# Optimization experiments

Hardware: AMD Instinct MI355X
Metric: run time of the kernel (lower is better)

Reference implementation:

```python
import jax, jax.numpy as jnp
import numpy as np

N_HEADS = 16
NEG = -1000000000.0  # masked_fill value from the original code


def setup_inputs() -> dict:
    key = jax.random.key(0)
    ks = jax.random.split(key, 7)
    D = 1024
    x = jax.random.normal(ks[0], (2, 2048, D), dtype=jnp.float32)
    s = 1.0 / np.sqrt(D)
    Wq = jax.random.normal(ks[1], (D, D), dtype=jnp.float32) * s
    bq = jax.random.normal(ks[2], (D,), dtype=jnp.float32) * 0.01
    Wk = jax.random.normal(ks[3], (D, D), dtype=jnp.float32) * s
    bk = jax.random.normal(ks[4], (D,), dtype=jnp.float32) * 0.01
    Wv = jax.random.normal(ks[5], (D, D), dtype=jnp.float32) * s
    bv = jax.random.normal(ks[6], (D,), dtype=jnp.float32) * 0.01
    return {"x": x, "Wq": Wq, "bq": bq, "Wk": Wk, "bk": bk, "Wv": Wv, "bv": bv}


def reference(x, Wq, bq, Wk, bk, Wv, bv):
    B, S, D = x.shape
    H = N_HEADS
    dh = D // H
    # nn.Linear: x @ W.T + b
    Q = (x @ Wq.T + bq).reshape(B, S, H, dh)
    K = (x @ Wk.T + bk).reshape(B, S, H, dh)
    V = (x @ Wv.T + bv).reshape(B, S, H, dh)
    # NOTE: original scales by sqrt(n_heads), not sqrt(d_head) -- faithful.
    scale = jnp.asarray(H, x.dtype) ** 0.5
    scores = jnp.einsum('bqhd,bkhd->bhqk', Q, K) / scale  # [B,H,S,S]
    # Original: mask = triu(ones, diag=1); scores.masked_fill(mask == 0, -1e9)
    # i.e. positions where the STRICT-UPPER mask is False (lower triangle incl.
    # diagonal) get -1e9. Faithful reproduction of that (buggy) behavior.
    triu = jnp.triu(jnp.ones((S, S), dtype=bool), k=1)  # [S,S]
    scores = jnp.where(triu[None, None, :, :], scores, jnp.asarray(NEG, x.dtype))
    probs = jax.nn.softmax(scores, axis=-1)
    # dropout is identity at inference
    out = jnp.einsum('bhqk,bkhd->bqhd', probs, V).reshape(B, S, D)
    return out
```

## Files before the change

### kernel.cpp

```cpp
#include <hip/hip_runtime.h>
#include <stdint.h>

typedef unsigned short u16;
typedef __attribute__((ext_vector_type(8))) short bf16x8;
typedef __attribute__((ext_vector_type(4))) float floatx4;

#define MFMA16(a, b, c) __builtin_amdgcn_mfma_f32_16x16x32_bf16(a, b, c, 0, 0, 0)
#define MEMFENCE asm volatile("" ::: "memory")

#if __has_builtin(__builtin_amdgcn_exp2f)
#define EXP2(x) __builtin_amdgcn_exp2f(x)
#else
#define EXP2(x) __expf(0.6931471805599453f * (x))
#endif

__device__ __forceinline__ u16 f2bf(float f) {
  unsigned u = __builtin_bit_cast(unsigned, f);
  return (u16)((u + 0x7FFFu + ((u >> 16) & 1u)) >> 16);
}
__device__ __forceinline__ u16 f2bf_hu(float f) {
  return (u16)((__builtin_bit_cast(unsigned, f) + 0x8000u) >> 16);
}
__device__ __forceinline__ float bf2f(u16 v) {
  return __builtin_bit_cast(float, (unsigned)v << 16);
}

__device__ __forceinline__ void glds16(void* lds, const void* g) {
  __builtin_amdgcn_global_load_lds((const __attribute__((address_space(1))) void*)g,
                                   (__attribute__((address_space(3))) void*)lds,
                                   16, 0, 0);
}

__global__ __launch_bounds__(256) void cvt_all(
    const float* __restrict__ x, const float* __restrict__ w0,
    const float* __restrict__ w1, const float* __restrict__ w2,
    u16* __restrict__ xb, u16* __restrict__ Wb) {
  const int bid = blockIdx.x;
  const float* src;
  u16* dst;
  int i;
  if (bid < 4096) {
    src = x; dst = xb; i = bid * 256 + threadIdx.x;
  } else {
    const int z = (bid - 4096) >> 10;
    src = (z == 0) ? w0 : (z == 1) ? w1 : w2;
    dst = Wb + (size_t)z * (1024 * 1024);
    i = ((bid - 4096) & 1023) * 256 + threadIdx.x;
  }
  float4 f = reinterpret_cast<const float4*>(src)[i];
  ushort4 o;
  o.x = f2bf(f.x); o.y = f2bf(f.y); o.z = f2bf(f.z); o.w = f2bf(f.w);
  reinterpret_cast<ushort4*>(dst)[i] = o;
}

__global__ __launch_bounds__(256, 3) void qkv_gemm(
    const u16* __restrict__ xb, const u16* __restrict__ Wb,
    const float* __restrict__ bq, const float* __restrict__ bk,
    const float* __restrict__ bv,
    u16* __restrict__ Qb, u16* __restrict__ Kb, u16* __restrict__ VTb) {
  __shared__ __attribute__((aligned(16))) u16 smem[2 * 128 * 64];
  u16* As = smem;
  u16* Bs = smem + 128 * 64;

  const int tid = threadIdx.x;
  const int w = tid >> 6, lane = tid & 63;
  const int lo = lane & 15, quad = lane >> 4;
  const int which = blockIdx.z;
  const int m0 = blockIdx.x * 128, n0 = blockIdx.y * 128;

  const u16* W = Wb + (size_t)which * (1024 * 1024);
  const int wm = (w >> 1) * 64, wn = (w & 1) * 64;

  floatx4 acc[4][4];
  for (int i = 0; i < 4; ++i)
    for (int j = 0; j < 4; ++j) acc[i][j] = (floatx4)0.f;

  const int arow = lane >> 3;
  const int aswz = ((lane & 7) ^ arow) * 8;

  for (int kt = 0; kt < 16; ++kt) {
    const int k0 = kt * 64;
    for (int j = 0; j < 4; ++j) {
      const int seg = w * 4 + j;
      glds16(As + seg * 512, xb + (size_t)(m0 + seg * 8 + arow) * 1024 + k0 + aswz);
      glds16(Bs + seg * 512, W + (size_t)(n0 + seg * 8 + arow) * 1024 + k0 + aswz);
    }
    __syncthreads();
    for (int kk = 0; kk < 2; ++kk) {
      const int swz = ((kk * 4 + quad) ^ (lo & 7)) * 8;
      bf16x8 af[4], bfr[4];
      for (int it = 0; it < 4; ++it)
        af[it] = *reinterpret_cast<const bf16x8*>(As + (wm + it * 16 + lo) * 64 + swz);
      for (int jt = 0; jt < 4; ++jt)
        bfr[jt] = *reinterpret_cast<const bf16x8*>(Bs + (wn + jt * 16 + lo) * 64 + swz);
      for (int it = 0; it < 4; ++it)
        for (int jt = 0; jt < 4; ++jt)
          acc[it][jt] = MFMA16(af[it], bfr[jt], acc[it][jt]);
    }
    __syncthreads();
  }

  const float* bias = (which == 0) ? bq : (which == 1) ? bk : bv;
  float bb[4];
  for (int jt = 0; jt < 4; ++jt) bb[jt] = bias[n0 + wn + jt * 16 + lo];
  const int b = m0 >> 11;

  if (which < 2) {
    const float scl = (which == 0) ? 0.36067376022224085f : 1.0f;
    u16* Tw = smem + w * (16 * 72);
    const int hblk = (n0 + wn) >> 6;
    u16* dst = ((which == 0) ? Qb : Kb) +
               ((size_t)(b * 16 + hblk) * 2048 + ((m0 & 2047) + wm)) * 64;
    for (int it = 0; it < 4; ++it) {
      for (int jt = 0; jt < 4; ++jt)
        for (int r = 0; r < 4; ++r) {
          const int m = quad * 4 + r, col = jt * 16 + lo;
          Tw[m * 72 + (((col >> 3) ^ (m & 7)) * 8) + (col & 7)] =
              f2bf((acc[it][jt][r] + bb[jt]) * scl);
        }
      MEMFENCE;
      for (int rd = 0; rd < 2; ++rd) {
        const int sr = rd * 8 + (lane >> 3), d8 = lane & 7;
        bf16x8 v = *reinterpret_cast<const bf16x8*>(Tw + sr * 72 + ((d8 ^ (sr & 7)) * 8));
        *reinterpret_cast<bf16x8*>(dst + (size_t)(it * 16 + sr) * 64 + d8 * 8) = v;
      }
      MEMFENCE;
    }
  } else {
    for (int pass = 0; pass < 2; ++pass) {
      if ((wm >> 6) == pass) {
        for (int it = 0; it < 4; ++it)
          for (int jt = 0; jt < 4; ++jt)
            for (int r = 0; r < 4; ++r) {
              const int n = wn + jt * 16 + lo;
              const int m = it * 16 + quad * 4 + r;
              smem[n * 72 + (((m >> 3) ^ (n & 7)) * 8) + (m & 7)] =
                  f2bf(acc[it][jt][r] + bb[jt]);
            }
      }
      __syncthreads();
      for (int rd = 0; rd < 4; ++rd) {
        const int n = (tid >> 3) + rd * 32, m8 = tid & 7;
        bf16x8 v = *reinterpret_cast<const bf16x8*>(smem + n * 72 + ((m8 ^ (n & 7)) * 8));
        const int ng = n0 + n, h = ng >> 6, d = ng & 63;
        const int s = (m0 & 2047) + pass * 64 + m8 * 8;
        *reinterpret_cast<bf16x8*>(VTb + ((size_t)(b * 16 + h) * 64 + d) * 2048 + s) = v;
      }
      __syncthreads();
    }
  }
}

__global__ __launch_bounds__(256, 4) void attn(
    const u16* __restrict__ Qb, const u16* __restrict__ Kb,
    const u16* __restrict__ VTb, float* __restrict__ out) {
  __shared__ __attribute__((aligned(16))) u16 Ks[2][64 * 64];
  __shared__ __attribute__((aligned(16))) u16 Vs[2][64 * 64];
  __shared__ __attribute__((aligned(16))) u16 Pt[4][16 * 64];

  const int L = blockIdx.x;
  const int bh = L & 31;
  const int j = L >> 5;
  const int g = j >> 3, r = j & 7;
  const int qi = (g == 0) ? r : (g == 1) ? 15 - r : (g == 2) ? 16 + r : 31 - r;
  const int kstart = qi;

  const int tid = threadIdx.x, w = tid >> 6, lane = tid & 63;
  const int lo = lane & 15, quad = lane >> 4;

  const u16* Qh = Qb + (size_t)bh * (2048 * 64);
  const u16* Kh = Kb + (size_t)bh * (2048 * 64);
  const u16* Vh = VTb + (size_t)bh * (64 * 2048);

  const int qrow = qi * 64 + w * 16 + lo;
  bf16x8 qf[2];
  qf[0] = *reinterpret_cast<const bf16x8*>(Qh + (size_t)qrow * 64 + quad * 8);
  qf[1] = *reinterpret_cast<const bf16x8*>(Qh + (size_t)qrow * 64 + 32 + quad * 8);

  float lrun = 0.f;
  floatx4 acc[4];
  for (int dt = 0; dt < 4; ++dt) acc[dt] = (floatx4)0.f;

  const int srow8 = lane >> 3, sblk = lane & 7;
  const int sswz = (sblk ^ srow8) * 8;

  for (int jj = 0; jj < 2; ++jj) {
    const int b8 = (w * 2 + jj) * 8;
    glds16(&Ks[0][b8 * 64], Kh + (size_t)(kstart * 64 + b8 + srow8) * 64 + sswz);
    glds16(&Vs[0][b8 * 64], Vh + (size_t)(b8 + srow8) * 2048 + kstart * 64 + sswz);
  }
  __syncthreads();

  for (int kt = kstart; kt < 32; ++kt) {
    const int cur = (kt - kstart) & 1, nxt = cur ^ 1;
    if (kt < 31)
      for (int jj = 0; jj < 2; ++jj) {
        const int b8 = (w * 2 + jj) * 8;
        glds16(&Ks[nxt][b8 * 64], Kh + (size_t)((kt + 1) * 64 + b8 + srow8) * 64 + sswz);
        glds16(&Vs[nxt][b8 * 64], Vh + (size_t)(b8 + srow8) * 2048 + (kt + 1) * 64 + sswz);
      }
    const u16* ksb = Ks[cur];
    const u16* vsb = Vs[cur];

    const bool maskp = (kt == kstart);

    floatx4 sc[4];
    for (int t = 0; t < 4; ++t) sc[t] = (floatx4)0.f;
    for (int kk = 0; kk < 2; ++kk) {
      const int swz = ((kk * 4 + quad) ^ (lo & 7)) * 8;
      for (int t = 0; t < 4; ++t) {
        bf16x8 ka = *reinterpret_cast<const bf16x8*>(ksb + (t * 16 + lo) * 64 + swz);
        sc[t] = MFMA16(ka, qf[kk], sc[t]);
      }
    }

    u16* ptw = &Pt[w][0];
    for (int t = 0; t < 4; ++t) {
      float p0 = EXP2(sc[t][0]), p1 = EXP2(sc[t][1]);
      float p2 = EXP2(sc[t][2]), p3 = EXP2(sc[t][3]);
      if (maskp) {
        const int key = kt * 64 + t * 16 + quad * 4;
        p0 = (key + 0 > qrow) ? p0 : 0.f;
        p1 = (key + 1 > qrow) ? p1 : 0.f;
        p2 = (key + 2 > qrow) ? p2 : 0.f;
        p3 = (key + 3 > qrow) ? p3 : 0.f;
      }
      lrun += (p0 + p1) + (p2 + p3);
      ushort4 pk;
      pk.x = f2bf_hu(p0); pk.y = f2bf_hu(p1);
      pk.z = f2bf_hu(p2); pk.w = f2bf_hu(p3);
      u16* pdst = ptw + lo * 64 +
                  (((2 * t + (quad >> 1)) ^ (lo & 7)) * 8) + (quad & 1) * 4;
      *reinterpret_cast<ushort4*>(pdst) = pk;
    }
    MEMFENCE;

    for (int kk = 0; kk < 2; ++kk) {
      const int pswz = ((kk * 4 + quad) ^ (lo & 7)) * 8;
      bf16x8 pb = *reinterpret_cast<const bf16x8*>(ptw + lo * 64 + pswz);
      for (int dt = 0; dt < 4; ++dt) {
        bf16x8 va = *reinterpret_cast<const bf16x8*>(vsb + (dt * 16 + lo) * 64 + pswz);
        acc[dt] = MFMA16(va, pb, acc[dt]);
      }
    }
    MEMFENCE;
    __syncthreads();
  }

  const int b = bh >> 4, hh = bh & 15;
  float l = lrun;
  l += __shfl_xor(l, 16);
  l += __shfl_xor(l, 32);
  if (l != 0.f) {
    const float rl = 1.f / l;
    float* op = out + ((size_t)(b * 2048 + qrow)) * 1024 + hh * 64 + quad * 4;
    for (int dt = 0; dt < 4; ++dt) {
      float4 o4;
      o4.x = acc[dt][0] * rl; o4.y = acc[dt][1] * rl;
      o4.z = acc[dt][2] * rl; o4.w = acc[dt][3] * rl;
      *reinterpret_cast<float4*>(op + dt * 16) = o4;
    }
  }
}

__global__ __launch_bounds__(256) void fix2047(const u16* __restrict__ VTb,
                                               float* __restrict__ out) {
  const int bh = blockIdx.x;
  const u16* Vh = VTb + (size_t)bh * (64 * 2048);
  const int t = threadIdx.x;
  const int d = t >> 2, j = t & 3;
  float s = 0.f;
  const u16* row = Vh + (size_t)d * 2048 + j * 512;
  for (int i = 0; i < 64; ++i) {
    bf16x8 v = *reinterpret_cast<const bf16x8*>(row + i * 8);
    for (int e = 0; e < 8; ++e) s += bf2f((u16)v[e]);
  }
  s += __shfl_xor(s, 1);
  s += __shfl_xor(s, 2);
  if (j == 0) {
    const int b = bh >> 4, h = bh & 15;
    out[((size_t)(b * 2048 + 2047)) * 1024 + h * 64 + d] = s * (1.f / 2048.f);
  }
}

extern "C" void kernel_launch(void* const* d_in, const int* in_sizes, int n_in,
                              void* d_out, int out_size, void* d_ws, size_t ws_size,
                              hipStream_t stream) {
  const float* x  = (const float*)d_in[0];
  const float* Wq = (const float*)d_in[1];
  const float* bq = (const float*)d_in[2];
  const float* Wk = (const float*)d_in[3];
  const float* bk = (const float*)d_in[4];
  const float* Wv = (const float*)d_in[5];
  const float* bv = (const float*)d_in[6];
  float* out = (float*)d_out;

  char* ws = (char*)d_ws;
  u16* xb  = (u16*)(ws);
  u16* Wb  = (u16*)(ws + (8u << 20));
  u16* Qb  = (u16*)(ws + (14u << 20));
  u16* Kb  = (u16*)(ws + (22u << 20));
  u16* VTb = (u16*)(ws + (30u << 20));

  cvt_all<<<7168, 256, 0, stream>>>(x, Wq, Wk, Wv, xb, Wb);
  qkv_gemm<<<dim3(32, 8, 3), 256, 0, stream>>>(xb, Wb, bq, bk, bv, Qb, Kb, VTb);
  attn<<<dim3(1024), 256, 0, stream>>>(Qb, Kb, VTb, out);
  fix2047<<<dim3(32), 256, 0, stream>>>(VTb, out);
}
```

Baseline: 151.5 us.

## Load V fragments directly from global into registers and fold fix2047 into attn

The V tile is no longer staged through shared memory. Each lane loads its MFMA A-operand fragments for V straight from global (L2) memory at the start of each key tile, which halves LDS usage and removes the V async copies. The separate fix2047 kernel becomes 32 extra blocks at the front of the attention grid, saving one launch. The cost is uncached per-lane global loads with 2048-element strides, issued without prefetch into the next iteration, so load latency may be exposed before the PV MFMAs.

```diff
diff --git a/kernel.cpp b/kernel.cpp
--- a/kernel.cpp
+++ b/kernel.cpp
@@ -155,12 +155,32 @@
     const u16* __restrict__ Qb, const u16* __restrict__ Kb,
     const u16* __restrict__ VTb, float* __restrict__ out) {
   __shared__ __attribute__((aligned(16))) u16 Ks[2][64 * 64];
-  __shared__ __attribute__((aligned(16))) u16 Vs[2][64 * 64];
   __shared__ __attribute__((aligned(16))) u16 Pt[4][16 * 64];
 
   const int L = blockIdx.x;
-  const int bh = L & 31;
-  const int j = L >> 5;
+  if (L < 32) {
+    const int bh = L;
+    const u16* Vh = VTb + (size_t)bh * (64 * 2048);
+    const int t = threadIdx.x;
+    const int d = t >> 2, jj = t & 3;
+    float s = 0.f;
+    const u16* row = Vh + (size_t)d * 2048 + jj * 512;
+    for (int i = 0; i < 64; ++i) {
+      bf16x8 v = *reinterpret_cast<const bf16x8*>(row + i * 8);
+      for (int e = 0; e < 8; ++e) s += bf2f((u16)v[e]);
+    }
+    s += __shfl_xor(s, 1);
+    s += __shfl_xor(s, 2);
+    if (jj == 0) {
+      const int b = bh >> 4, h = bh & 15;
+      out[((size_t)(b * 2048 + 2047)) * 1024 + h * 64 + d] = s * (1.f / 2048.f);
+    }
+    return;
+  }
+
+  const int M = L - 32;
+  const int bh = M & 31;
+  const int j = M >> 5;
   const int g = j >> 3, r = j & 7;
   const int qi = (g == 0) ? r : (g == 1) ? 15 - r : (g == 2) ? 16 + r : 31 - r;
   const int kstart = qi;
@@ -187,20 +207,26 @@
   for (int jj = 0; jj < 2; ++jj) {
     const int b8 = (w * 2 + jj) * 8;
     glds16(&Ks[0][b8 * 64], Kh + (size_t)(kstart * 64 + b8 + srow8) * 64 + sswz);
-    glds16(&Vs[0][b8 * 64], Vh + (size_t)(b8 + srow8) * 2048 + kstart * 64 + sswz);
   }
   __syncthreads();
+
+  const u16* Vbase = Vh + (size_t)lo * 2048 + quad * 8;
 
   for (int kt = kstart; kt < 32; ++kt) {
     const int cur = (kt - kstart) & 1, nxt = cur ^ 1;
+
+    bf16x8 vfrag[2][4];
+    for (int kk = 0; kk < 2; ++kk)
+      for (int dt = 0; dt < 4; ++dt)
+        vfrag[kk][dt] = *reinterpret_cast<const bf16x8*>(
+            Vbase + (size_t)dt * (16 * 2048) + kt * 64 + kk * 32);
+
     if (kt < 31)
       for (int jj = 0; jj < 2; ++jj) {
         const int b8 = (w * 2 + jj) * 8;
         glds16(&Ks[nxt][b8 * 64], Kh + (size_t)((kt + 1) * 64 + b8 + srow8) * 64 + sswz);
-        glds16(&Vs[nxt][b8 * 64], Vh + (size_t)(b8 + srow8) * 2048 + (kt + 1) * 64 + sswz);
       }
     const u16* ksb = Ks[cur];
-    const u16* vsb = Vs[cur];
 
     const bool maskp = (kt == kstart);
 
@@ -238,10 +264,8 @@
     for (int kk = 0; kk < 2; ++kk) {
       const int pswz = ((kk * 4 + quad) ^ (lo & 7)) * 8;
       bf16x8 pb = *reinterpret_cast<const bf16x8*>(ptw + lo * 64 + pswz);
-      for (int dt = 0; dt < 4; ++dt) {
-        bf16x8 va = *reinterpret_cast<const bf16x8*>(vsb + (dt * 16 + lo) * 64 + pswz);
-        acc[dt] = MFMA16(va, pb, acc[dt]);
-      }
+      for (int dt = 0; dt < 4; ++dt)
+        acc[dt] = MFMA16(vfrag[kk][dt], pb, acc[dt]);
     }
     MEMFENCE;
     __syncthreads();
@@ -263,26 +287,6 @@
   }
 }
 
-__global__ __launch_bounds__(256) void fix2047(const u16* __restrict__ VTb,
-                                               float* __restrict__ out) {
-  const int bh = blockIdx.x;
-  const u16* Vh = VTb + (size_t)bh * (64 * 2048);
-  const int t = threadIdx.x;
-  const int d = t >> 2, j = t & 3;
-  float s = 0.f;
-  const u16* row = Vh + (size_t)d * 2048 + j * 512;
-  for (int i = 0; i < 64; ++i) {
-    bf16x8 v = *reinterpret_cast<const bf16x8*>(row + i * 8);
-    for (int e = 0; e < 8; ++e) s += bf2f((u16)v[e]);
-  }
-  s += __shfl_xor(s, 1);
-  s += __shfl_xor(s, 2);
-  if (j == 0) {
-    const int b = bh >> 4, h = bh & 15;
-    out[((size_t)(b * 2048 + 2047)) * 1024 + h * 64 + d] = s * (1.f / 2048.f);
-  }
-}
-
 extern "C" void kernel_launch(void* const* d_in, const int* in_sizes, int n_in,
                               void* d_out, int out_size, void* d_ws, size_t ws_size,
                               hipStream_t stream) {
@@ -304,6 +308,5 @@
 
   cvt_all<<<7168, 256, 0, stream>>>(x, Wq, Wk, Wv, xb, Wb);
   qkv_gemm<<<dim3(32, 8, 3), 256, 0, stream>>>(xb, Wb, bq, bk, bv, Qb, Kb, VTb);
-  attn<<<dim3(1024), 256, 0, stream>>>(Qb, Kb, VTb, out);
-  fix2047<<<dim3(32), 256, 0, stream>>>(VTb, out);
-}
+  attn<<<dim3(1056), 256, 0, stream>>>(Qb, Kb, VTb, out);
+}
```

Result: slower. 188.7 us (+24.6%).
